# Kernel optimization log

Hardware: AMD Instinct MI355X
Metric: run time of the kernel (lower is better)

Reference implementation:

```python
import jax, jax.numpy as jnp
import numpy as np

D = 2048          # hidden_size
H = 16            # num attention heads
HD = D // H       # head_dim = 128
DFF = 8192        # intermediate_size
DLCA = 4096       # d_lca = 2*hidden_size
EPS = 1e-6
LAM, TAU, DT, NSTEPS = 0.1, 0.1, 0.01, 10
ROPE_THETA = 10000.0


def rmsnorm(x, w):
    v = jnp.mean(x.astype(jnp.float32) ** 2, axis=-1, keepdims=True)
    return (x * jax.lax.rsqrt(v + EPS)).astype(x.dtype) * w


def rope_cos_sin(seq_len, dtype):
    inv_freq = 1.0 / (ROPE_THETA ** (jnp.arange(0, HD, 2, dtype=jnp.float32) / HD))
    t = jnp.arange(seq_len, dtype=jnp.float32)
    freqs = jnp.outer(t, inv_freq)              # [S, HD/2]
    emb = jnp.concatenate([freqs, freqs], -1)   # [S, HD]
    return jnp.cos(emb).astype(dtype), jnp.sin(emb).astype(dtype)


def rotate_half(x):
    x1, x2 = jnp.split(x, 2, axis=-1)
    return jnp.concatenate([-x2, x1], axis=-1)


def setup_inputs() -> dict:
    key = jax.random.key(0)
    ks = jax.random.split(key, 10)
    s = 0.02
    return {
        "hidden_states": jax.random.normal(ks[0], (2, 2048, D), jnp.float32),
        "w_ln_in": jnp.ones((D,), jnp.float32),
        "w_ln_lca": jnp.ones((D,), jnp.float32),
        "w_ln_post": jnp.ones((D,), jnp.float32),
        "Wq": jax.random.normal(ks[1], (D, D), jnp.float32) * s,
        "Wk": jax.random.normal(ks[2], (D, D), jnp.float32) * s,
        "Wv": jax.random.normal(ks[3], (D, D), jnp.float32) * s,
        "Wo": jax.random.normal(ks[4], (D, D), jnp.float32) * s,
        "W_lca": jax.random.normal(ks[5], (D, DLCA), jnp.float32) * s,
        "W_gate": jax.random.normal(ks[6], (D, DFF), jnp.float32) * s,
        "W_up": jax.random.normal(ks[7], (D, DFF), jnp.float32) * s,
        "W_down": jax.random.normal(ks[8], (DFF, D), jnp.float32) * s,
    }


def reference(hidden_states, w_ln_in, w_ln_lca, w_ln_post, Wq, Wk, Wv, Wo,
              W_lca, W_gate, W_up, W_down):
    B, S, _ = hidden_states.shape
    residual = hidden_states

    # --- causal self-attention with RoPE ---
    h = rmsnorm(hidden_states, w_ln_in)
    q = (h @ Wq).reshape(B, S, H, HD).transpose(0, 2, 1, 3)  # [B,H,S,HD]
    k = (h @ Wk).reshape(B, S, H, HD).transpose(0, 2, 1, 3)
    v = (h @ Wv).reshape(B, S, H, HD).transpose(0, 2, 1, 3)
    cos, sin = rope_cos_sin(S, h.dtype)
    q = q * cos + rotate_half(q) * sin
    k = k * cos + rotate_half(k) * sin
    scores = jnp.einsum('bhqd,bhkd->bhqk', q, k) / jnp.sqrt(jnp.asarray(HD, h.dtype))
    causal = jnp.tril(jnp.ones((S, S), bool))
    scores = jnp.where(causal, scores, jnp.finfo(scores.dtype).min)
    probs = jax.nn.softmax(scores, axis=-1)
    attn = jnp.einsum('bhqk,bhkd->bhqd', probs, v)
    attn = attn.transpose(0, 2, 1, 3).reshape(B, S, D) @ Wo
    h = residual + attn

    # --- LCA: project up, 10-step lateral-competition recurrence, project back ---
    hn = rmsnorm(h, w_ln_lca)
    xf = hn.reshape(-1, D)                       # [B*S, D]
    b = xf @ W_lca                               # [B*S, DLCA]
    G = W_lca.T @ W_lca                          # [DLCA, DLCA]
    G = G - jnp.diag(jnp.diag(G))                # zero diagonal (self-inhibition)
    u = jnp.zeros_like(b)
    for _ in range(NSTEPS):
        a = jax.nn.relu(u - LAM)
        u = u + DT * ((b - a @ G - u) / TAU)
    a = jax.nn.relu(u - LAM)
    h = (a @ W_lca.T).reshape(B, S, D)           # LCA REPLACES the residual stream

    # --- MLP (SwiGLU) with residual ---
    residual = h
    m = rmsnorm(h, w_ln_post)
    mlp = (jax.nn.silu(m @ W_gate) * (m @ W_up)) @ W_down
    return residual + mlp
```

## Files before the change

kernel.cpp:

```cpp
#include <hip/hip_runtime.h>
#include <hip/hip_fp8.h>

typedef short bf16x8 __attribute__((ext_vector_type(8)));
typedef float f32x4 __attribute__((ext_vector_type(4)));
typedef long long ll;

__device__ __forceinline__ unsigned short f2bf(float f) {
    union { float f; unsigned u; } v; v.f = f;
    unsigned u = v.u;
    unsigned r = (u + 0x7FFFu + ((u >> 16) & 1u)) >> 16;
    return (unsigned short)r;
}
__device__ __forceinline__ float bf2f(unsigned short h) {
    union { unsigned u; float f; } v; v.u = ((unsigned)h) << 16; return v.f;
}
__device__ __forceinline__ unsigned char f2fp8(float f) {
    __hip_fp8_e4m3 q(f);
    return (unsigned char)q.__x;
}

typedef const __attribute__((address_space(1))) void gas_void;
typedef __attribute__((address_space(3))) void las_void;
__device__ __forceinline__ void gll16(const void* g, void* l) {
    __builtin_amdgcn_global_load_lds((gas_void*)g, (las_void*)l, 16, 0, 0);
}

__global__ __launch_bounds__(256) void gemm_bf16(
    const unsigned short* __restrict__ A, ll lda, ll sAz,
    const unsigned short* __restrict__ B, ll ldb, ll sBz,
    void* __restrict__ C, ll ldc, ll sCz,
    int M, int N, int K,
    float alpha, int mode, int causal,
    const float* __restrict__ res)
{
    __shared__ unsigned short sA[2][4096];
    __shared__ unsigned short sB[2][4096];
    const int n0 = blockIdx.x * 128;
    const int m0 = blockIdx.y * 128;
    if (causal && n0 > m0) return;
    const int z = blockIdx.z;

    const unsigned short* Ab = A + (ll)z * sAz + (ll)m0 * lda;
    const unsigned short* Bb = B + (ll)z * sBz + (ll)n0 * ldb;

    const int t    = threadIdx.x;
    const int lane = t & 63;
    const int w    = t >> 6, wm = w >> 1, wn = w & 1;
    const int m16  = lane & 15, quad = lane >> 4;

    const int r0 = t >> 2, cs = t & 3;
    const int r1 = r0 + 64;
    const int c0 = cs ^ ((r0 >> 1) & 3);
    const int c1 = cs ^ ((r1 >> 1) & 3);
    const ll a_off0 = (ll)r0 * lda + c0 * 8;
    const ll a_off1 = (ll)r1 * lda + c1 * 8;
    const ll b_off0 = (ll)r0 * ldb + c0 * 8;
    const ll b_off1 = (ll)r1 * ldb + c1 * 8;
    const int dst = t * 8;

    int aoff[4], boff[4];
#pragma unroll
    for (int mi = 0; mi < 4; mi++) {
        int rr = wm * 64 + mi * 16 + m16;
        aoff[mi] = rr * 32 + ((quad ^ ((rr >> 1) & 3)) << 3);
    }
#pragma unroll
    for (int ni = 0; ni < 4; ni++) {
        int rr = wn * 64 + ni * 16 + m16;
        boff[ni] = rr * 32 + ((quad ^ ((rr >> 1) & 3)) << 3);
    }

    f32x4 acc[4][4];
#pragma unroll
    for (int i = 0; i < 4; i++)
#pragma unroll
        for (int j = 0; j < 4; j++) acc[i][j] = (f32x4){0.f, 0.f, 0.f, 0.f};

    gll16(Ab + a_off0, sA[0] + dst);
    gll16(Ab + a_off1, sA[0] + 2048 + dst);
    gll16(Bb + b_off0, sB[0] + dst);
    gll16(Bb + b_off1, sB[0] + 2048 + dst);
    __syncthreads();

    for (int kt = 0; kt < K; kt += 32) {
        const int cur = (kt >> 5) & 1;
        if (kt + 32 < K) {
            const int nxt = cur ^ 1;
            gll16(Ab + a_off0 + kt + 32, sA[nxt] + dst);
            gll16(Ab + a_off1 + kt + 32, sA[nxt] + 2048 + dst);
            gll16(Bb + b_off0 + kt + 32, sB[nxt] + dst);
            gll16(Bb + b_off1 + kt + 32, sB[nxt] + 2048 + dst);
        }
        bf16x8 af[4], bg[4];
#pragma unroll
        for (int mi = 0; mi < 4; mi++) af[mi] = *(const bf16x8*)(sA[cur] + aoff[mi]);
#pragma unroll
        for (int ni = 0; ni < 4; ni++) bg[ni] = *(const bf16x8*)(sB[cur] + boff[ni]);
#pragma unroll
        for (int mi = 0; mi < 4; mi++)
#pragma unroll
            for (int ni = 0; ni < 4; ni++)
                acc[mi][ni] = __builtin_amdgcn_mfma_f32_16x16x32_bf16(
                    af[mi], bg[ni], acc[mi][ni], 0, 0, 0);
        __syncthreads();
    }

    const ll czoff = (ll)z * sCz;
#pragma unroll
    for (int mi = 0; mi < 4; mi++) {
#pragma unroll
        for (int ni = 0; ni < 4; ni++) {
#pragma unroll
            for (int r = 0; r < 4; r++) {
                int row = m0 + wm * 64 + mi * 16 + quad * 4 + r;
                int col = n0 + wn * 64 + ni * 16 + m16;
                ll idx = czoff + (ll)row * ldc + col;
                float v = acc[mi][ni][r] * alpha;
                if (mode == 0) {
                    ((float*)C)[idx] = res ? (v + res[idx]) : v;
                } else if (mode == 1) {
                    ((unsigned short*)C)[idx] = f2bf(v);
                } else {
                    ((unsigned char*)C)[idx] = (row == col) ? (unsigned char)0 : f2fp8(v);
                }
            }
        }
    }
}

__global__ __launch_bounds__(256) void gemm_fp8(
    const unsigned char* __restrict__ A, ll lda,
    const unsigned char* __restrict__ B, ll ldb,
    int M, int N, int K, float alpha, int mode,
    unsigned short* __restrict__ uu, const unsigned short* __restrict__ cc,
    void* __restrict__ Out)
{
    __shared__ unsigned char sA[2][8192];
    __shared__ unsigned char sB[2][8192];
    const int n0 = blockIdx.x * 128;
    const int m0 = blockIdx.y * 128;

    const unsigned char* Ab = A + (ll)m0 * lda;
    const unsigned char* Bb = B + (ll)n0 * ldb;

    const int t    = threadIdx.x;
    const int lane = t & 63;
    const int w    = t >> 6, wm = w >> 1, wn = w & 1;
    const int m16  = lane & 15, quad = lane >> 4;

    const int r0 = t >> 2, cs = t & 3;
    const int r1 = r0 + 64;
    const int c0 = cs ^ ((r0 >> 1) & 3);
    const int c1 = cs ^ ((r1 >> 1) & 3);
    const ll a_off0 = (ll)r0 * lda + c0 * 16;
    const ll a_off1 = (ll)r1 * lda + c1 * 16;
    const ll b_off0 = (ll)r0 * ldb + c0 * 16;
    const ll b_off1 = (ll)r1 * ldb + c1 * 16;
    const int dst = t * 16;

    int aoff[4][2], boff[4][2];
#pragma unroll
    for (int mi = 0; mi < 4; mi++) {
        int rr = wm * 64 + mi * 16 + m16;
#pragma unroll
        for (int kh = 0; kh < 2; kh++) {
            int ch = kh * 2 + (quad >> 1);
            aoff[mi][kh] = rr * 64 + ((ch ^ ((rr >> 1) & 3)) << 4) + ((quad & 1) << 3);
        }
    }
#pragma unroll
    for (int ni = 0; ni < 4; ni++) {
        int rr = wn * 64 + ni * 16 + m16;
#pragma unroll
        for (int kh = 0; kh < 2; kh++) {
            int ch = kh * 2 + (quad >> 1);
            boff[ni][kh] = rr * 64 + ((ch ^ ((rr >> 1) & 3)) << 4) + ((quad & 1) << 3);
        }
    }

    f32x4 acc[4][4];
#pragma unroll
    for (int i = 0; i < 4; i++)
#pragma unroll
        for (int j = 0; j < 4; j++) acc[i][j] = (f32x4){0.f, 0.f, 0.f, 0.f};

    gll16(Ab + a_off0, sA[0] + dst);
    gll16(Ab + a_off1, sA[0] + 4096 + dst);
    gll16(Bb + b_off0, sB[0] + dst);
    gll16(Bb + b_off1, sB[0] + 4096 + dst);
    __syncthreads();

    for (int kt = 0; kt < K; kt += 64) {
        const int cur = (kt >> 6) & 1;
        if (kt + 64 < K) {
            const int nxt = cur ^ 1;
            gll16(Ab + a_off0 + kt + 64, sA[nxt] + dst);
            gll16(Ab + a_off1 + kt + 64, sA[nxt] + 4096 + dst);
            gll16(Bb + b_off0 + kt + 64, sB[nxt] + dst);
            gll16(Bb + b_off1 + kt + 64, sB[nxt] + 4096 + dst);
        }
#pragma unroll
        for (int kh = 0; kh < 2; kh++) {
            long long af[4], bg[4];
#pragma unroll
            for (int mi = 0; mi < 4; mi++)
                af[mi] = *(const long long*)(sA[cur] + aoff[mi][kh]);
#pragma unroll
            for (int ni = 0; ni < 4; ni++)
                bg[ni] = *(const long long*)(sB[cur] + boff[ni][kh]);
#pragma unroll
            for (int mi = 0; mi < 4; mi++)
#pragma unroll
                for (int ni = 0; ni < 4; ni++)
                    acc[mi][ni] = __builtin_amdgcn_mfma_f32_16x16x32_fp8_fp8(
                        af[mi], bg[ni], acc[mi][ni], 0, 0, 0);
        }
        __syncthreads();
    }

#pragma unroll
    for (int mi = 0; mi < 4; mi++) {
#pragma unroll
        for (int ni = 0; ni < 4; ni++) {
#pragma unroll
            for (int r = 0; r < 4; r++) {
                int row = m0 + wm * 64 + mi * 16 + quad * 4 + r;
                int col = n0 + wn * 64 + ni * 16 + m16;
                ll idx = (ll)row * N + col;
                float v = acc[mi][ni][r] * alpha;
                float un = 0.9f * bf2f(uu[idx]) + bf2f(cc[idx]) - v;
                uu[idx] = f2bf(un);
                float a = fmaxf(un - 0.1f, 0.0f);
                if (mode == 3) ((unsigned char*)Out)[idx] = f2fp8(a * 8.0f);
                else           ((unsigned short*)Out)[idx] = f2bf(a);
            }
        }
    }
}


__global__ void wtrans_k(const float* __restrict__ in, unsigned short* __restrict__ out,
                         int R, int C) {
    __shared__ float tile[32][33];
    ll bx = (ll)blockIdx.x * 32, by = (ll)blockIdx.y * 32;
    int tx = threadIdx.x & 31, ty = threadIdx.x >> 5;
#pragma unroll
    for (int i = ty; i < 32; i += 8) tile[i][tx] = in[(by + i) * C + bx + tx];
    __syncthreads();
#pragma unroll
    for (int i = ty; i < 32; i += 8) out[(bx + i) * R + by + tx] = f2bf(tile[tx][i]);
}

__global__ void conv4_k(const float* __restrict__ in, unsigned short* __restrict__ out, ll n) {
    ll i = ((ll)blockIdx.x * 256 + threadIdx.x) * 4;
    if (i >= n) return;
    float4 v = *(const float4*)(in + i);
    out[i] = f2bf(v.x); out[i + 1] = f2bf(v.y); out[i + 2] = f2bf(v.z); out[i + 3] = f2bf(v.w);
}

__global__ void rmsnorm_k(const float* __restrict__ in, const float* __restrict__ w,
                          unsigned short* __restrict__ out) {
    int row = blockIdx.x, t = threadIdx.x;
    const float* x = in + (ll)row * 2048;
    float v[8]; float s = 0.f;
#pragma unroll
    for (int i = 0; i < 8; i++) { v[i] = x[t + i * 256]; s += v[i] * v[i]; }
#pragma unroll
    for (int o = 32; o > 0; o >>= 1) s += __shfl_xor(s, o, 64);
    __shared__ float rs[4];
    if ((t & 63) == 0) rs[t >> 6] = s;
    __syncthreads();
    s = (rs[0] + rs[1] + rs[2] + rs[3]) * (1.0f / 2048.0f);
    float sc = rsqrtf(s + 1e-6f);
    unsigned short* o_ = out + (ll)row * 2048;
#pragma unroll
    for (int i = 0; i < 8; i++) o_[t + i * 256] = f2bf(v[i] * sc * w[t + i * 256]);
}

__global__ void rope_k(unsigned short* __restrict__ q, unsigned short* __restrict__ k) {
    int idx = blockIdx.x * 256 + threadIdx.x;
    int j = idx & 63;
    int h = (idx >> 6) & 15;
    int row = idx >> 10;
    int s = row & 2047;
    float f = __expf(-(float)j * 0.14391156831212783f);
    float ang = (float)s * f;
    float sn, cs;
    sincosf(ang, &sn, &cs);
    ll base = (ll)row * 2048 + h * 128 + j;
    float x1 = bf2f(q[base]), x2 = bf2f(q[base + 64]);
    q[base]      = f2bf(x1 * cs - x2 * sn);
    q[base + 64] = f2bf(x2 * cs + x1 * sn);
    x1 = bf2f(k[base]); x2 = bf2f(k[base + 64]);
    k[base]      = f2bf(x1 * cs - x2 * sn);
    k[base + 64] = f2bf(x2 * cs + x1 * sn);
}

__global__ void vtrans_k(const unsigned short* __restrict__ in, unsigned short* __restrict__ out) {
    __shared__ unsigned short tile[32][33];
    int z = blockIdx.z, b = z >> 4, h = z & 15;
    const unsigned short* ib = in + (ll)b * 4194304 + h * 128;
    unsigned short* ob = out + (ll)z * 262144;
    int bx = blockIdx.x * 32, by = blockIdx.y * 32;
    int tx = threadIdx.x & 31, ty = threadIdx.x >> 5;
#pragma unroll
    for (int i = ty; i < 32; i += 8) tile[i][tx] = ib[(ll)(by + i) * 2048 + bx + tx];
    __syncthreads();
#pragma unroll
    for (int i = ty; i < 32; i += 8) ob[(ll)(bx + i) * 2048 + by + tx] = tile[tx][i];
}

__global__ void softmax_k(unsigned short* __restrict__ sc) {
    int q = blockIdx.x, z = blockIdx.y, t = threadIdx.x;
    unsigned short* row = sc + (ll)z * 4194304 + (ll)q * 2048;
    float x[8]; float m = -1e30f;
#pragma unroll
    for (int i = 0; i < 8; i++) {
        int kk = t + i * 256;
        x[i] = (kk <= q) ? bf2f(row[kk]) : -1e30f;
        m = fmaxf(m, x[i]);
    }
#pragma unroll
    for (int o = 32; o > 0; o >>= 1) m = fmaxf(m, __shfl_xor(m, o, 64));
    __shared__ float rm[4];
    if ((t & 63) == 0) rm[t >> 6] = m;
    __syncthreads();
    m = fmaxf(fmaxf(rm[0], rm[1]), fmaxf(rm[2], rm[3]));
    float s = 0.f;
#pragma unroll
    for (int i = 0; i < 8; i++) {
        int kk = t + i * 256;
        float e = (kk <= q) ? __expf(x[i] - m) : 0.0f;
        x[i] = e; s += e;
    }
#pragma unroll
    for (int o = 32; o > 0; o >>= 1) s += __shfl_xor(s, o, 64);
    __shared__ float rsum[4];
    if ((t & 63) == 0) rsum[t >> 6] = s;
    __syncthreads();
    s = rsum[0] + rsum[1] + rsum[2] + rsum[3];
    float inv = 1.0f / s;
#pragma unroll
    for (int i = 0; i < 8; i++) row[t + i * 256] = f2bf(x[i] * inv);
}

__global__ void lca_init_k(const unsigned short* __restrict__ c, unsigned short* __restrict__ u,
                           unsigned char* __restrict__ a) {
    ll i = ((ll)blockIdx.x * 256 + threadIdx.x) * 4;
#pragma unroll
    for (int j = 0; j < 4; j++) {
        unsigned short cv = c[i + j];
        u[i + j] = cv;
        a[i + j] = f2fp8(fmaxf(bf2f(cv) - 0.1f, 0.f) * 8.0f);
    }
}

__global__ void swiglu_k(unsigned short* __restrict__ g, const unsigned short* __restrict__ u) {
    ll i = ((ll)blockIdx.x * 256 + threadIdx.x) * 4;
#pragma unroll
    for (int j = 0; j < 4; j++) {
        float x = bf2f(g[i + j]);
        float y = bf2f(u[i + j]);
        float sil = x / (1.0f + __expf(-x));
        g[i + j] = f2bf(sil * y);
    }
}

extern "C" void kernel_launch(void* const* d_in, const int* in_sizes, int n_in,
                              void* d_out, int out_size, void* d_ws, size_t ws_size,
                              hipStream_t stream) {
    (void)in_sizes; (void)n_in; (void)out_size; (void)ws_size;
    const float* X        = (const float*)d_in[0];
    const float* wln_in   = (const float*)d_in[1];
    const float* wln_lca  = (const float*)d_in[2];
    const float* wln_post = (const float*)d_in[3];
    const float* Wq   = (const float*)d_in[4];
    const float* Wk   = (const float*)d_in[5];
    const float* Wv   = (const float*)d_in[6];
    const float* Wo   = (const float*)d_in[7];
    const float* Wlca = (const float*)d_in[8];
    const float* Wg   = (const float*)d_in[9];
    const float* Wu   = (const float*)d_in[10];
    const float* Wd   = (const float*)d_in[11];
    float* out = (float*)d_out;

    char* ws = (char*)d_ws;
    unsigned short* WqT = (unsigned short*)(ws);
    unsigned short* WkT = WqT + 4194304;
    unsigned short* WvT = WqT + 2 * 4194304;
    unsigned short* WoT = WqT + 3 * 4194304;
    unsigned short* WgT = WqT;
    unsigned short* WlcaT = (unsigned short*)(ws + 33554432);
    unsigned short* Wlcab = WlcaT + 8388608;
    unsigned short* WuT   = WlcaT;
    unsigned short* h_bf = (unsigned short*)(ws + 67108864);
    char* pool = ws + 83886080;
    unsigned short* qb     = (unsigned short*)(pool);
    unsigned short* kb     = (unsigned short*)(pool + 16777216);
    unsigned short* vb     = (unsigned short*)(pool + 33554432);
    unsigned short* VT     = (unsigned short*)(pool + 50331648);
    unsigned short* attn   = (unsigned short*)(pool + 67108864);
    unsigned short* scores = (unsigned short*)(pool + 83886080);
    float* h1              = (float*)(pool + 150994944);
    unsigned short* cbuf   = (unsigned short*)(pool);
    unsigned short* ubuf   = (unsigned short*)(pool + 33554432);
    unsigned char* a8_0    = (unsigned char*)(pool + 67108864);
    unsigned char* a8_1    = (unsigned char*)(pool + 83886080);
    unsigned short* abf    = (unsigned short*)(pool + 100663296);
    unsigned char* Gf8     = (unsigned char*)(pool + 134217728);
    float* h2              = (float*)(pool + 150994944);
    unsigned short* gate   = (unsigned short*)(pool);
    unsigned short* up     = (unsigned short*)(pool + 67108864);
    unsigned short* WdT    = (unsigned short*)(pool + 201326592);

    dim3 blk(256);
    auto gemm = [&](const unsigned short* A, ll lda, ll sAz,
                    const unsigned short* Bt, ll ldb, ll sBz,
                    void* C, ll ldc, ll sCz,
                    int M, int N, int K, int Z,
                    float alpha, int mode, int causal, const float* res) {
        dim3 g(N / 128, M / 128, Z);
        gemm_bf16<<<g, blk, 0, stream>>>(A, lda, sAz, Bt, ldb, sBz, C, ldc, sCz,
                                         M, N, K, alpha, mode, causal, res);
    };

    wtrans_k<<<dim3(64, 64), blk, 0, stream>>>(Wq, WqT, 2048, 2048);
    wtrans_k<<<dim3(64, 64), blk, 0, stream>>>(Wk, WkT, 2048, 2048);
    wtrans_k<<<dim3(64, 64), blk, 0, stream>>>(Wv, WvT, 2048, 2048);
    wtrans_k<<<dim3(64, 64), blk, 0, stream>>>(Wo, WoT, 2048, 2048);
    wtrans_k<<<dim3(128, 64), blk, 0, stream>>>(Wlca, WlcaT, 2048, 4096);
    conv4_k<<<8192, blk, 0, stream>>>(Wlca, Wlcab, 8388608LL);

    rmsnorm_k<<<4096, blk, 0, stream>>>(X, wln_in, h_bf);
    gemm(h_bf, 2048, 0, WqT, 2048, 0, qb, 2048, 0, 4096, 2048, 2048, 1, 1.f, 1, 0, nullptr);
    gemm(h_bf, 2048, 0, WkT, 2048, 0, kb, 2048, 0, 4096, 2048, 2048, 1, 1.f, 1, 0, nullptr);
    gemm(h_bf, 2048, 0, WvT, 2048, 0, vb, 2048, 0, 4096, 2048, 2048, 1, 1.f, 1, 0, nullptr);
    rope_k<<<16384, blk, 0, stream>>>(qb, kb);
    vtrans_k<<<dim3(4, 64, 32), blk, 0, stream>>>(vb, VT);
    for (int c = 0; c < 4; c++) {
        int b = c >> 1, h0 = (c & 1) * 8;
        const unsigned short* qbase = qb + (ll)b * 4194304 + h0 * 128;
        const unsigned short* kbase = kb + (ll)b * 4194304 + h0 * 128;
        gemm(qbase, 2048, 128, kbase, 2048, 128, scores, 2048, 4194304LL,
             2048, 2048, 128, 8, 0.08838834764831845f, 1, 1, nullptr);
        softmax_k<<<dim3(2048, 8), blk, 0, stream>>>(scores);
        const unsigned short* vtb = VT + (ll)(b * 16 + h0) * 262144;
        unsigned short* ab = attn + (ll)b * 4194304 + h0 * 128;
        gemm(scores, 2048, 4194304LL, vtb, 2048, 262144LL, ab, 2048, 128,
             2048, 128, 2048, 8, 1.f, 1, 0, nullptr);
    }
    gemm(attn, 2048, 0, WoT, 2048, 0, h1, 2048, 0, 4096, 2048, 2048, 1, 1.f, 0, 0, X);

    rmsnorm_k<<<4096, blk, 0, stream>>>(h1, wln_lca, h_bf);
    gemm(WlcaT, 2048, 0, WlcaT, 2048, 0, Gf8, 4096, 0, 4096, 4096, 2048, 1, 16.f, 2, 0, nullptr);
    gemm(h_bf, 2048, 0, WlcaT, 2048, 0, cbuf, 4096, 0, 4096, 4096, 2048, 1, 0.1f, 1, 0, nullptr);
    lca_init_k<<<16384, blk, 0, stream>>>(cbuf, ubuf, a8_0);
    unsigned char* acur = a8_0; unsigned char* anext = a8_1;
    for (int i = 0; i < 9; i++) {
        int mode = (i < 8) ? 3 : 4;
        void* outp = (i < 8) ? (void*)anext : (void*)abf;
        gemm_fp8<<<dim3(32, 32), blk, 0, stream>>>(
            acur, 4096, Gf8, 4096, 4096, 4096, 4096,
            0.1f / 128.0f, mode, ubuf, cbuf, outp);
        unsigned char* tmp = acur; acur = anext; anext = tmp;
    }
    gemm(abf, 4096, 0, Wlcab, 4096, 0, h2, 2048, 0, 4096, 2048, 4096, 1, 1.f, 0, 0, nullptr);

    wtrans_k<<<dim3(256, 64), blk, 0, stream>>>(Wg, WgT, 2048, 8192);
    wtrans_k<<<dim3(256, 64), blk, 0, stream>>>(Wu, WuT, 2048, 8192);
    wtrans_k<<<dim3(64, 256), blk, 0, stream>>>(Wd, WdT, 8192, 2048);
    rmsnorm_k<<<4096, blk, 0, stream>>>(h2, wln_post, h_bf);
    gemm(h_bf, 2048, 0, WgT, 2048, 0, gate, 8192, 0, 4096, 8192, 2048, 1, 1.f, 1, 0, nullptr);
    gemm(h_bf, 2048, 0, WuT, 2048, 0, up, 8192, 0, 4096, 8192, 2048, 1, 1.f, 1, 0, nullptr);
    swiglu_k<<<32768, blk, 0, stream>>>(gate, up);
    gemm(gate, 8192, 0, WdT, 8192, 0, out, 2048, 0, 4096, 2048, 8192, 1, 1.f, 0, 0, h2);
}
```

Measured before the change: 3.324 ms.

## Add large-tile 4-stage pipelined GEMM kernel for dense projections

Adds a new bf16 MFMA GEMM kernel with 512 threads, 256x256 or 128x256 tiles, a 4-deep LDS ring fed by global_load_lds with swizzled layout, explicit vmcnt waits, and an XCD-aware block remap. All the large dense projections (QKV, O, LCA Gram and projections, MLP) now use it instead of the 128x128 double-buffered kernel. The aim is higher data reuse per tile and better hiding of load latency. In exchange it uses more LDS and registers per block, and small grids (e.g. the 128x256 tiles on 4096x2048) may leave CUs underused.

```diff
diff --git a/kernel.cpp b/kernel.cpp
--- a/kernel.cpp
+++ b/kernel.cpp
@@ -23,6 +23,148 @@
 typedef __attribute__((address_space(3))) void las_void;
 __device__ __forceinline__ void gll16(const void* g, void* l) {
     __builtin_amdgcn_global_load_lds((gas_void*)g, (las_void*)l, 16, 0, 0);
+}
+
+template<int N> __device__ __forceinline__ void wb() {
+    __builtin_amdgcn_sched_barrier(0);
+    if constexpr (N == 8)      asm volatile("s_waitcnt vmcnt(8)" ::: "memory");
+    else if constexpr (N == 6) asm volatile("s_waitcnt vmcnt(6)" ::: "memory");
+    else if constexpr (N == 4) asm volatile("s_waitcnt vmcnt(4)" ::: "memory");
+    else if constexpr (N == 3) asm volatile("s_waitcnt vmcnt(3)" ::: "memory");
+    else                       asm volatile("s_waitcnt vmcnt(0)" ::: "memory");
+    __builtin_amdgcn_s_barrier();
+    __builtin_amdgcn_sched_barrier(0);
+}
+
+template<int BM, int BN>
+__global__ __launch_bounds__(512, 2) void gemm_big_k(
+    const unsigned short* __restrict__ A, ll lda,
+    const unsigned short* __restrict__ B, ll ldb,
+    void* __restrict__ C, ll ldc,
+    int K, float alpha, int mode, const float* __restrict__ res)
+{
+    constexpr int MI  = BM / 32;
+    constexpr int NI  = BN / 64;
+    constexpr int LPA = BM / 128;
+    constexpr int LPB = BN / 128;
+    constexpr int LPT = LPA + LPB;
+    __shared__ unsigned short sA[4 * BM * 32];
+    __shared__ unsigned short sB[4 * BN * 32];
+
+    const int nwg = gridDim.x * gridDim.y;
+    int id = blockIdx.y * gridDim.x + blockIdx.x;
+    {
+        int q = nwg >> 3, r = nwg & 7, x = id & 7, bb = id >> 3;
+        id = (x < r ? x * (q + 1) : r * (q + 1) + (x - r) * q) + bb;
+    }
+    const int n0 = (id % gridDim.x) * BN;
+    const int m0 = (id / gridDim.x) * BM;
+
+    const unsigned short* Ab = A + (ll)m0 * lda;
+    const unsigned short* Bb = B + (ll)n0 * ldb;
+
+    const int t    = threadIdx.x;
+    const int lane = t & 63;
+    const int w    = t >> 6, wm = w >> 2, wn = w & 3;
+    const int m16  = lane & 15, quad = lane >> 4;
+
+    int srcA[LPA], srcB[LPB], dstA[LPA], dstB[LPB];
+#pragma unroll
+    for (int j = 0; j < LPA; j++) {
+        int d = j * 8192 + t * 16;
+        int p = d >> 7;
+        int e = ((d >> 4) & 7) ^ (p & 7);
+        int row = (p << 1) | (e >> 2);
+        srcA[j] = row * (int)lda + (e & 3) * 8;
+        dstA[j] = j * 4096 + t * 8;
+    }
+#pragma unroll
+    for (int j = 0; j < LPB; j++) {
+        int d = j * 8192 + t * 16;
+        int p = d >> 7;
+        int e = ((d >> 4) & 7) ^ (p & 7);
+        int row = (p << 1) | (e >> 2);
+        srcB[j] = row * (int)ldb + (e & 3) * 8;
+        dstB[j] = j * 4096 + t * 8;
+    }
+
+    int aoff[MI], boff[NI];
+#pragma unroll
+    for (int mi = 0; mi < MI; mi++) {
+        int r = wm * (BM / 2) + mi * 16 + m16;
+        int c = (((r & 1) << 2) | quad) ^ ((r >> 1) & 7);
+        aoff[mi] = (r >> 1) * 64 + (c << 3);
+    }
+#pragma unroll
+    for (int ni = 0; ni < NI; ni++) {
+        int r = wn * 64 + ni * 16 + m16;
+        int c = (((r & 1) << 2) | quad) ^ ((r >> 1) & 7);
+        boff[ni] = (r >> 1) * 64 + (c << 3);
+    }
+
+    f32x4 acc[MI][NI];
+#pragma unroll
+    for (int i = 0; i < MI; i++)
+#pragma unroll
+        for (int j = 0; j < NI; j++) acc[i][j] = (f32x4){0.f, 0.f, 0.f, 0.f};
+
+    auto stage = [&](int tile) {
+        const int s  = tile & 3;
+        const int kt = tile << 5;
+#pragma unroll
+        for (int j = 0; j < LPA; j++)
+            gll16(Ab + srcA[j] + kt, sA + s * (BM * 32) + dstA[j]);
+#pragma unroll
+        for (int j = 0; j < LPB; j++)
+            gll16(Bb + srcB[j] + kt, sB + s * (BN * 32) + dstB[j]);
+    };
+
+    const int nT = K >> 5;
+    stage(0); stage(1); stage(2);
+    wb<2 * LPT>();
+
+    for (int T = 0; T < nT; ++T) {
+        if (T + 3 < nT) stage(T + 3);
+        const unsigned short* bufA = sA + (T & 3) * (BM * 32);
+        const unsigned short* bufB = sB + (T & 3) * (BN * 32);
+        bf16x8 af[MI], bg[NI];
+#pragma unroll
+        for (int ni = 0; ni < NI; ni++) bg[ni] = *(const bf16x8*)(bufB + boff[ni]);
+#pragma unroll
+        for (int mi = 0; mi < MI; mi++) af[mi] = *(const bf16x8*)(bufA + aoff[mi]);
+        __builtin_amdgcn_s_setprio(1);
+#pragma unroll
+        for (int mi = 0; mi < MI; mi++)
+#pragma unroll
+            for (int ni = 0; ni < NI; ni++)
+                acc[mi][ni] = __builtin_amdgcn_mfma_f32_16x16x32_bf16(
+                    af[mi], bg[ni], acc[mi][ni], 0, 0, 0);
+        __builtin_amdgcn_s_setprio(0);
+        if (T + 4 <= nT)      wb<2 * LPT>();
+        else if (T + 3 == nT) wb<LPT>();
+        else if (T + 2 == nT) wb<0>();
+    }
+
+#pragma unroll
+    for (int mi = 0; mi < MI; mi++) {
+#pragma unroll
+        for (int ni = 0; ni < NI; ni++) {
+#pragma unroll
+            for (int r4 = 0; r4 < 4; r4++) {
+                int row = m0 + wm * (BM / 2) + mi * 16 + quad * 4 + r4;
+                int col = n0 + wn * 64 + ni * 16 + m16;
+                ll idx = (ll)row * ldc + col;
+                float v = acc[mi][ni][r4] * alpha;
+                if (mode == 0) {
+                    ((float*)C)[idx] = res ? (v + res[idx]) : v;
+                } else if (mode == 1) {
+                    ((unsigned short*)C)[idx] = f2bf(v);
+                } else {
+                    ((unsigned char*)C)[idx] = (row == col) ? (unsigned char)0 : f2fp8(v);
+                }
+            }
+        }
+    }
 }
 
 __global__ __launch_bounds__(256) void gemm_bf16(
@@ -423,6 +565,19 @@
         gemm_bf16<<<g, blk, 0, stream>>>(A, lda, sAz, Bt, ldb, sBz, C, ldc, sCz,
                                          M, N, K, alpha, mode, causal, res);
     };
+    auto gemm_big = [&](const unsigned short* A, ll lda, const unsigned short* Bt, ll ldb,
+                        void* C, ll ldc, int M, int N, int K, float alpha, int mode,
+                        const float* res, int wide) {
+        if (wide) {
+            dim3 g(N / 256, M / 256);
+            gemm_big_k<256, 256><<<g, dim3(512), 0, stream>>>(A, lda, Bt, ldb, C, ldc,
+                                                              K, alpha, mode, res);
+        } else {
+            dim3 g(N / 256, M / 128);
+            gemm_big_k<128, 256><<<g, dim3(512), 0, stream>>>(A, lda, Bt, ldb, C, ldc,
+                                                              K, alpha, mode, res);
+        }
+    };
 
     wtrans_k<<<dim3(64, 64), blk, 0, stream>>>(Wq, WqT, 2048, 2048);
     wtrans_k<<<dim3(64, 64), blk, 0, stream>>>(Wk, WkT, 2048, 2048);
@@ -432,9 +587,9 @@
     conv4_k<<<8192, blk, 0, stream>>>(Wlca, Wlcab, 8388608LL);
 
     rmsnorm_k<<<4096, blk, 0, stream>>>(X, wln_in, h_bf);
-    gemm(h_bf, 2048, 0, WqT, 2048, 0, qb, 2048, 0, 4096, 2048, 2048, 1, 1.f, 1, 0, nullptr);
-    gemm(h_bf, 2048, 0, WkT, 2048, 0, kb, 2048, 0, 4096, 2048, 2048, 1, 1.f, 1, 0, nullptr);
-    gemm(h_bf, 2048, 0, WvT, 2048, 0, vb, 2048, 0, 4096, 2048, 2048, 1, 1.f, 1, 0, nullptr);
+    gemm_big(h_bf, 2048, WqT, 2048, qb, 2048, 4096, 2048, 2048, 1.f, 1, nullptr, 0);
+    gemm_big(h_bf, 2048, WkT, 2048, kb, 2048, 4096, 2048, 2048, 1.f, 1, nullptr, 0);
+    gemm_big(h_bf, 2048, WvT, 2048, vb, 2048, 4096, 2048, 2048, 1.f, 1, nullptr, 0);
     rope_k<<<16384, blk, 0, stream>>>(qb, kb);
     vtrans_k<<<dim3(4, 64, 32), blk, 0, stream>>>(vb, VT);
     for (int c = 0; c < 4; c++) {
@@ -449,11 +604,11 @@
         gemm(scores, 2048, 4194304LL, vtb, 2048, 262144LL, ab, 2048, 128,
              2048, 128, 2048, 8, 1.f, 1, 0, nullptr);
     }
-    gemm(attn, 2048, 0, WoT, 2048, 0, h1, 2048, 0, 4096, 2048, 2048, 1, 1.f, 0, 0, X);
+    gemm_big(attn, 2048, WoT, 2048, h1, 2048, 4096, 2048, 2048, 1.f, 0, X, 0);
 
     rmsnorm_k<<<4096, blk, 0, stream>>>(h1, wln_lca, h_bf);
-    gemm(WlcaT, 2048, 0, WlcaT, 2048, 0, Gf8, 4096, 0, 4096, 4096, 2048, 1, 16.f, 2, 0, nullptr);
-    gemm(h_bf, 2048, 0, WlcaT, 2048, 0, cbuf, 4096, 0, 4096, 4096, 2048, 1, 0.1f, 1, 0, nullptr);
+    gemm_big(WlcaT, 2048, WlcaT, 2048, Gf8, 4096, 4096, 4096, 2048, 16.f, 2, nullptr, 1);
+    gemm_big(h_bf, 2048, WlcaT, 2048, cbuf, 4096, 4096, 4096, 2048, 0.1f, 1, nullptr, 1);
     lca_init_k<<<16384, blk, 0, stream>>>(cbuf, ubuf, a8_0);
     unsigned char* acur = a8_0; unsigned char* anext = a8_1;
     for (int i = 0; i < 9; i++) {
@@ -464,14 +619,14 @@
             0.1f / 128.0f, mode, ubuf, cbuf, outp);
         unsigned char* tmp = acur; acur = anext; anext = tmp;
     }
-    gemm(abf, 4096, 0, Wlcab, 4096, 0, h2, 2048, 0, 4096, 2048, 4096, 1, 1.f, 0, 0, nullptr);
+    gemm_big(abf, 4096, Wlcab, 4096, h2, 2048, 4096, 2048, 4096, 1.f, 0, nullptr, 0);
 
     wtrans_k<<<dim3(256, 64), blk, 0, stream>>>(Wg, WgT, 2048, 8192);
     wtrans_k<<<dim3(256, 64), blk, 0, stream>>>(Wu, WuT, 2048, 8192);
     wtrans_k<<<dim3(64, 256), blk, 0, stream>>>(Wd, WdT, 8192, 2048);
     rmsnorm_k<<<4096, blk, 0, stream>>>(h2, wln_post, h_bf);
-    gemm(h_bf, 2048, 0, WgT, 2048, 0, gate, 8192, 0, 4096, 8192, 2048, 1, 1.f, 1, 0, nullptr);
-    gemm(h_bf, 2048, 0, WuT, 2048, 0, up, 8192, 0, 4096, 8192, 2048, 1, 1.f, 1, 0, nullptr);
+    gemm_big(h_bf, 2048, WgT, 2048, gate, 8192, 4096, 8192, 2048, 1.f, 1, nullptr, 1);
+    gemm_big(h_bf, 2048, WuT, 2048, up, 8192, 4096, 8192, 2048, 1.f, 1, nullptr, 1);
     swiglu_k<<<32768, blk, 0, stream>>>(gate, up);
-    gemm(gate, 8192, 0, WdT, 8192, 0, out, 2048, 0, 4096, 2048, 8192, 1, 1.f, 0, 0, h2);
-}
+    gemm_big(gate, 8192, WdT, 8192, out, 2048, 4096, 2048, 8192, 1.f, 0, h2, 0);
+}
```

Result: slower. 3.677 ms (+10.6%).
